# Kernel tuning notes

Hardware: AMD Instinct MI355X
Metric: run time of the kernel (lower is better)

The kernel has to match this reference:

```python
import jax, jax.numpy as jnp
import numpy as np

NUM_HEADS = 8
BN_EPS = 1e-5


def setup_inputs() -> dict:
    key = jax.random.key(0)
    ks = jax.random.split(key, 8)
    B, Ct, Cs, H, W, E = 8, 256, 128, 32, 32, 256
    s = 0.05  # small init scale to keep softmax logits reasonable
    return {
        "tgt": jax.random.normal(ks[0], (B, Ct, H, W), jnp.float32),
        "src": jax.random.normal(ks[1], (B, Cs, H, W), jnp.float32),
        "kv_w": jax.random.normal(ks[2], (E, Cs), jnp.float32) * s,
        "in_proj_w": jax.random.normal(ks[3], (3 * E, E), jnp.float32) * s,
        "in_proj_b": jnp.zeros((3 * E,), jnp.float32),
        "out_proj_w": jax.random.normal(ks[4], (E, E), jnp.float32) * s,
        "out_proj_b": jnp.zeros((E,), jnp.float32),
        "fuse_w": jax.random.normal(ks[5], (Ct, E), jnp.float32) * s,
        "bn_gamma": jnp.ones((Ct,), jnp.float32),
        "bn_beta": jnp.zeros((Ct,), jnp.float32),
        "bn_mean": jnp.zeros((Ct,), jnp.float32),
        "bn_var": jnp.ones((Ct,), jnp.float32),
    }


def reference(tgt, src, kv_w, in_proj_w, in_proj_b, out_proj_w, out_proj_b,
              fuse_w, bn_gamma, bn_beta, bn_mean, bn_var):
    B, Ct, H, W = tgt.shape
    E = kv_w.shape[0]
    nH = NUM_HEADS
    hd = E // nH

    # q_proj is Identity (C_tgt == embed_dim); flatten spatial to tokens [B, Q, E]
    q_seq = tgt.reshape(B, Ct, H * W).transpose(0, 2, 1)
    # kv_proj: 1x1 conv == channel matmul; then flatten to [B, K, E]
    kv_map = jnp.einsum('bchw,ec->behw', src, kv_w)
    k_seq = kv_map.reshape(B, E, H * W).transpose(0, 2, 1)

    # nn.MultiheadAttention: packed in-projection
    Wq, Wk, Wv = in_proj_w[:E], in_proj_w[E:2 * E], in_proj_w[2 * E:]
    bq, bk, bv = in_proj_b[:E], in_proj_b[E:2 * E], in_proj_b[2 * E:]
    qp = (q_seq @ Wq.T + bq).reshape(B, -1, nH, hd).transpose(0, 2, 1, 3)  # [B,h,Q,d]
    kp = (k_seq @ Wk.T + bk).reshape(B, -1, nH, hd).transpose(0, 2, 1, 3)  # [B,h,K,d]
    vp = (k_seq @ Wv.T + bv).reshape(B, -1, nH, hd).transpose(0, 2, 1, 3)  # [B,h,K,d]

    scores = jnp.einsum('bhqd,bhkd->bhqk', qp, kp) / jnp.sqrt(jnp.float32(hd))
    attn = jax.nn.softmax(scores, axis=-1)  # [B,h,Q,K] (non-flash explicit path)

    ctx = jnp.einsum('bhqk,bhkd->bhqd', attn, vp)
    ctx = ctx.transpose(0, 2, 1, 3).reshape(B, -1, E)  # [B,Q,E]
    out_seq = ctx @ out_proj_w.T + out_proj_b

    # cached spatial key-attention map: mean over heads and queries -> [B,1,Hk,Wk]
    attn_map = attn.mean(axis=(1, 2)).reshape(B, 1, H, W)

    # back to map, fuse: 1x1 conv -> BN(eval) -> SiLU, then residual add
    out_map = out_seq.transpose(0, 2, 1).reshape(B, E, H, W)
    fused = jnp.einsum('behw,ce->bchw', out_map, fuse_w)
    inv = bn_gamma / jnp.sqrt(bn_var + BN_EPS)
    bn = (fused - bn_mean[None, :, None, None]) * inv[None, :, None, None] \
         + bn_beta[None, :, None, None]
    y = tgt + bn * jax.nn.sigmoid(bn)  # SiLU
    return y, attn_map
```

## Files before the change

kernel.cpp:

```cpp
#include <hip/hip_runtime.h>
#include <hip/hip_bf16.h>

typedef unsigned short u16;
typedef unsigned int u32;
typedef __attribute__((ext_vector_type(8))) short short8;
typedef __attribute__((ext_vector_type(4))) float f32x4;
typedef __attribute__((ext_vector_type(4))) unsigned short u16x4;
typedef __attribute__((ext_vector_type(4))) int i32x4;

static __device__ __forceinline__ u16 f2bf(float x) {
  __hip_bfloat16 b = __float2bfloat16(x);
  return *reinterpret_cast<u16*>(&b);
}
static __device__ __forceinline__ u32 fbits(float x) {
  union { float f; u32 u; } v; v.f = x; return v.u;
}
static __device__ __forceinline__ u32 pk_trunc(float lo, float hi) {
  return __builtin_amdgcn_perm(fbits(hi), fbits(lo), 0x07060302u);
}
static __device__ __forceinline__ void gl2lds16(const u16* g, u16* l) {
  __builtin_amdgcn_global_load_lds(
      (const __attribute__((address_space(1))) void*)g,
      (__attribute__((address_space(3))) void*)l, 16, 0, 0);
}

#define QSCALE2 (0.17677669529663687f * 1.4426950408889634f)

__global__ __launch_bounds__(256) void prep_xpose(
    const float* __restrict__ in_proj_w, const float* __restrict__ in_proj_b,
    const float* __restrict__ kv_w, const float* __restrict__ fuse_w,
    const float* __restrict__ out_proj_w, const float* __restrict__ out_proj_b,
    const float* __restrict__ gamma, const float* __restrict__ beta,
    const float* __restrict__ mean, const float* __restrict__ var,
    const float* __restrict__ tgt, const float* __restrict__ src,
    u16* __restrict__ WqB, u16* __restrict__ WkvB, u16* __restrict__ M2B,
    float* __restrict__ qbias, float2* __restrict__ bnpk,
    u16* __restrict__ tgtT, u16* __restrict__ srcT,
    float* __restrict__ attn_out) {
  if (blockIdx.x >= 1537) {
    int i = (blockIdx.x - 1537) * 256 + threadIdx.x;
    attn_out[i] = 0.f;
    return;
  }
  if (blockIdx.x < 769) {
    int idx = blockIdx.x * 256 + threadIdx.x;
    if (idx < 65536) {
      WqB[idx] = f2bf(in_proj_w[idx] * QSCALE2);
    } else if (idx < 131072) {
      int i = idx - 65536;
      int m = i >> 7, c = i & 127;
      const float* wrow = in_proj_w + (size_t)(256 + m) * 256;
      float s = 0.f;
      for (int e2 = 0; e2 < 256; ++e2) s += wrow[e2] * kv_w[e2 * 128 + c];
      WkvB[i] = f2bf(s);
    } else if (idx < 196608) {
      int i = idx - 131072;
      int c = i >> 8, e2 = i & 255;
      float s = 0.f;
      for (int e = 0; e < 256; ++e)
        s += fuse_w[c * 256 + e] * out_proj_w[e * 256 + e2];
      M2B[i] = f2bf(s);
    } else if (idx < 196864) {
      int c = idx - 196608;
      float fbv = 0.f;
      for (int e = 0; e < 256; ++e) fbv += fuse_w[c * 256 + e] * out_proj_b[e];
      float inv = gamma[c] * rsqrtf(var[c] + 1e-5f);
      bnpk[c] = make_float2(inv, (fbv - mean[c]) * inv + beta[c]);
      qbias[c] = in_proj_b[c] * QSCALE2;
    }
    return;
  }
  int i0 = blockIdx.x - 769;
  int b = i0 / 96, rem = i0 % 96;
  int by = rem >> 4, sb = (rem & 15) * 64;
  const float* X;
  u16* XT;
  int C, cb;
  if (by < 4) {
    X = tgt + (size_t)b * 256 * 1024;
    XT = tgtT + (size_t)b * 1024 * 256;
    C = 256;
    cb = by * 64;
  } else {
    X = src + (size_t)b * 128 * 1024;
    XT = srcT + (size_t)b * 1024 * 128;
    C = 128;
    cb = (by - 4) * 64;
  }
  int t = threadIdx.x;
  int c = cb + (t >> 4) * 4;
  int s = sb + (t & 15) * 4;
  const float* Xp = X + (size_t)c * 1024 + s;
  float4 r0 = *(const float4*)(Xp);
  float4 r1 = *(const float4*)(Xp + 1024);
  float4 r2 = *(const float4*)(Xp + 2048);
  float4 r3 = *(const float4*)(Xp + 3072);
  u16* XTp = XT + (size_t)s * C + c;
  u16x4 o;
  o[0] = f2bf(r0.x); o[1] = f2bf(r1.x); o[2] = f2bf(r2.x); o[3] = f2bf(r3.x);
  *(u16x4*)(XTp) = o;
  o[0] = f2bf(r0.y); o[1] = f2bf(r1.y); o[2] = f2bf(r2.y); o[3] = f2bf(r3.y);
  *(u16x4*)(XTp + C) = o;
  o[0] = f2bf(r0.z); o[1] = f2bf(r1.z); o[2] = f2bf(r2.z); o[3] = f2bf(r3.z);
  *(u16x4*)(XTp + 2 * C) = o;
  o[0] = f2bf(r0.w); o[1] = f2bf(r1.w); o[2] = f2bf(r2.w); o[3] = f2bf(r3.w);
  *(u16x4*)(XTp + 3 * C) = o;
}

__global__ __launch_bounds__(256, 4) void qkv_gemm(
    const u16* __restrict__ tgtT, const u16* __restrict__ srcT,
    const u16* __restrict__ WqB, const u16* __restrict__ WkvB,
    const float* __restrict__ qbias, const float* __restrict__ bkv,
    u16* __restrict__ QB, u16* __restrict__ KB, u16* __restrict__ VB) {
  __shared__ __align__(16) u16 Wl[64 * 32];
  __shared__ __align__(16) u16 Xl[128 * 32];
  int b = blockIdx.z, my = blockIdx.y, n0 = blockIdx.x * 128;
  bool isQ = my < 4;
  int m0 = isQ ? my * 64 : (my - 4) * 64;
  int Kd = isQ ? 256 : 128;
  const u16* Wp = isQ ? WqB : WkvB;
  const u16* Xp = isQ ? tgtT + (size_t)b * 1024 * 256
                      : srcT + (size_t)b * 1024 * 128;
  int t = threadIdx.x, wave = t >> 6, lane = t & 63;
  int lq = lane & 15, quad = lane >> 4;
  int srow = t >> 2, sseg = t & 3;
  f32x4 acc[4][2];
#pragma unroll
  for (int mt = 0; mt < 4; ++mt)
#pragma unroll
    for (int nt = 0; nt < 2; ++nt) acc[mt][nt] = (f32x4){0.f, 0.f, 0.f, 0.f};

  for (int k0 = 0; k0 < Kd; k0 += 32) {
    __syncthreads();
    gl2lds16(&Wp[(size_t)(m0 + srow) * Kd + k0 + sseg * 8], &Wl[wave * 512]);
    gl2lds16(&Xp[(size_t)(n0 + srow) * Kd + k0 + sseg * 8], &Xl[wave * 512]);
    gl2lds16(&Xp[(size_t)(n0 + 64 + srow) * Kd + k0 + sseg * 8],
             &Xl[2048 + wave * 512]);
    __syncthreads();
    short8 af[4], bf[2];
#pragma unroll
    for (int mt = 0; mt < 4; ++mt)
      af[mt] = *(const short8*)&Wl[(mt * 16 + lq) * 32 + quad * 8];
#pragma unroll
    for (int nt = 0; nt < 2; ++nt)
      bf[nt] = *(const short8*)&Xl[(wave * 32 + nt * 16 + lq) * 32 + quad * 8];
#pragma unroll
    for (int mt = 0; mt < 4; ++mt)
#pragma unroll
      for (int nt = 0; nt < 2; ++nt)
        acc[mt][nt] = __builtin_amdgcn_mfma_f32_16x16x32_bf16(af[mt], bf[nt],
                                                              acc[mt][nt], 0, 0, 0);
  }
  if (isQ) {
#pragma unroll
    for (int mt = 0; mt < 4; ++mt) {
      int e = m0 + mt * 16 + quad * 4;
      f32x4 bi = *(const f32x4*)&qbias[e];
      int hh = e >> 5, d0 = e & 31;
#pragma unroll
      for (int nt = 0; nt < 2; ++nt) {
        int n = n0 + wave * 32 + nt * 16 + lq;
        u16x4 pk;
#pragma unroll
        for (int r = 0; r < 4; ++r) pk[r] = f2bf(acc[mt][nt][r] + bi[r]);
        *(u16x4*)&QB[((size_t)(b * 8 + hh) * 1024 + n) * 32 + d0] = pk;
      }
    }
  } else {
#pragma unroll
    for (int mt = 0; mt < 4; ++mt) {
      int m = m0 + mt * 16 + quad * 4;
      f32x4 bi = *(const f32x4*)&bkv[m];
#pragma unroll
      for (int nt = 0; nt < 2; ++nt) {
        int n = n0 + wave * 32 + nt * 16 + lq;
        if (m < 256) {
          int hh = m >> 5, d = m & 31;
          u16x4 pk;
#pragma unroll
          for (int r = 0; r < 4; ++r) pk[r] = f2bf(acc[mt][nt][r] + bi[r]);
          *(u16x4*)&KB[((size_t)(b * 8 + hh) * 1024 + n) * 32 + d] = pk;
        } else {
          int e = m - 256;
#pragma unroll
          for (int r = 0; r < 4; ++r)
            VB[((size_t)b * 256 + e + r) * 1024 + n] = f2bf(acc[mt][nt][r] + bi[r]);
        }
      }
    }
  }
}

__global__ __launch_bounds__(256, 4) void attn_passA(
    const u16* __restrict__ QB, const u16* __restrict__ KB,
    const u16* __restrict__ VB, u16* __restrict__ ctxB,
    float* __restrict__ linv_ws) {
  __shared__ __align__(16) u16 Klds[256 * 32];
  __shared__ __align__(16) u16 Vlds[8 * 1056];
  int bidx = blockIdx.x;
  int pair = bidx & 63, q0 = (bidx >> 6) * 64;
  int b = pair >> 3, h = pair & 7;
  int t = threadIdx.x, wave = t >> 6, lane = t & 63;
  int lq = lane & 15, quad = lane >> 4;
  int srow = t >> 2, sseg = t & 3;

  const u16* Qb = QB + (size_t)pair * 1024 * 32;
  const u16* Kb = KB + (size_t)pair * 1024 * 32;
  const u16* Vb = VB + (size_t)(b * 256 + h * 32) * 1024;

  int myq = q0 + wave * 16 + lq;
  short8 qf = *(const short8*)(Qb + (size_t)myq * 32 + quad * 8);

  const f32x4 zf = (f32x4){0.f, 0.f, 0.f, 0.f};
  f32x4 O0 = zf, O1 = zf;
  float lsum = 0.f;
  int keyA = ((lq >> 2) << 3) | (lq & 3);

  for (int c0 = 0; c0 < 1024; c0 += 256) {
    __syncthreads();
#pragma unroll
    for (int i = 0; i < 4; ++i)
      gl2lds16(Kb + (size_t)(c0 + i * 64 + srow) * 32 + sseg * 8,
               &Klds[i * 2048 + wave * 512]);
#pragma unroll
    for (int i = 0; i < 2; ++i) {
      int g = wave * 2 + i;
#pragma unroll
      for (int j = 0; j < 2; ++j) {
        int d = g * 4 + j * 2 + (lane >> 5);
        gl2lds16(Vb + (size_t)d * 1024 + c0 + (lane & 31) * 8,
                 &Vlds[g * 1056 + j * 512]);
      }
    }
    __syncthreads();
#pragma unroll
    for (int pr = 0; pr < 8; ++pr) {
      short8 kf0 = *(const short8*)&Klds[(pr * 32 + keyA) * 32 + quad * 8];
      short8 kf1 = *(const short8*)&Klds[(pr * 32 + keyA + 4) * 32 + quad * 8];
      f32x4 s0 = __builtin_amdgcn_mfma_f32_16x16x32_bf16(kf0, qf, zf, 0, 0, 0);
      f32x4 s1 = __builtin_amdgcn_mfma_f32_16x16x32_bf16(kf1, qf, zf, 0, 0, 0);
      f32x4 e0, e1;
#pragma unroll
      for (int r = 0; r < 4; ++r) {
        e0[r] = exp2f(s0[r]);
        e1[r] = exp2f(s1[r]);
      }
      lsum += (e0[0] + e0[1]) + (e0[2] + e0[3]) +
              (e1[0] + e1[1]) + (e1[2] + e1[3]);
      i32x4 pi;
      pi[0] = (int)pk_trunc(e0[0], e0[1]);
      pi[1] = (int)pk_trunc(e0[2], e0[3]);
      pi[2] = (int)pk_trunc(e1[0], e1[1]);
      pi[3] = (int)pk_trunc(e1[2], e1[3]);
      short8 pf = *(short8*)&pi;
      short8 vf0 = *(const short8*)&Vlds[(lq >> 2) * 1056 + (lq & 3) * 256 +
                                         pr * 32 + quad * 8];
      short8 vf1 = *(const short8*)&Vlds[(4 + (lq >> 2)) * 1056 + (lq & 3) * 256 +
                                         pr * 32 + quad * 8];
      O0 = __builtin_amdgcn_mfma_f32_16x16x32_bf16(vf0, pf, O0, 0, 0, 0);
      O1 = __builtin_amdgcn_mfma_f32_16x16x32_bf16(vf1, pf, O1, 0, 0, 0);
    }
  }

  lsum += __shfl_xor(lsum, 16);
  lsum += __shfl_xor(lsum, 32);
  float linv = 1.f / lsum;

  u16x4 pk0, pk1;
#pragma unroll
  for (int r = 0; r < 4; ++r) {
    pk0[r] = f2bf(O0[r] * linv);
    pk1[r] = f2bf(O1[r] * linv);
  }
  u16* crow = ctxB + ((size_t)b * 1024 + myq) * 256 + h * 32 + quad * 4;
  *(u16x4*)crow = pk0;
  *(u16x4*)(crow + 16) = pk1;
  if (quad == 0) linv_ws[(size_t)pair * 1024 + myq] = linv;
}

__global__ __launch_bounds__(256, 4) void colsum_kernel(
    const u16* __restrict__ QB, const u16* __restrict__ KB,
    const float* __restrict__ linv_ws, float* __restrict__ attn_out) {
  __shared__ __align__(16) u16 Klds[64 * 32];
  int bidx = blockIdx.x;
  int pair = bidx & 63, k0 = (bidx >> 6) * 64;
  int b = pair >> 3;
  int t = threadIdx.x, wave = t >> 6, lane = t & 63;
  int lq = lane & 15, quad = lane >> 4;
  int srow = t >> 2, sseg = t & 3;

  const u16* Qb = QB + (size_t)pair * 1024 * 32;
  const u16* Kb = KB + (size_t)pair * 1024 * 32;
  const float* lvp = linv_ws + (size_t)pair * 1024;

  gl2lds16(Kb + (size_t)(k0 + srow) * 32 + sseg * 8, &Klds[wave * 512]);
  __syncthreads();

  short8 kf[4];
#pragma unroll
  for (int nt = 0; nt < 4; ++nt)
    kf[nt] = *(const short8*)&Klds[(nt * 16 + lq) * 32 + quad * 8];

  const f32x4 zf = (f32x4){0.f, 0.f, 0.f, 0.f};
  float cs[4] = {0.f, 0.f, 0.f, 0.f};
  for (int g = 0; g < 16; ++g) {
    int qg = g * 64 + wave * 16;
    short8 qf = *(const short8*)(Qb + (size_t)(qg + lq) * 32 + quad * 8);
    f32x4 lv = *(const f32x4*)&lvp[qg + quad * 4];
#pragma unroll
    for (int nt = 0; nt < 4; ++nt) {
      f32x4 s = __builtin_amdgcn_mfma_f32_16x16x32_bf16(qf, kf[nt], zf, 0, 0, 0);
      cs[nt] += exp2f(s[0]) * lv[0] + exp2f(s[1]) * lv[1] +
                exp2f(s[2]) * lv[2] + exp2f(s[3]) * lv[3];
    }
  }
#pragma unroll
  for (int nt = 0; nt < 4; ++nt) {
    float v = cs[nt];
    v += __shfl_xor(v, 16);
    v += __shfl_xor(v, 32);
    if (quad == 0)
      atomicAdd(&attn_out[b * 1024 + k0 + nt * 16 + lq], v * (1.f / 8192.f));
  }
}

__global__ __launch_bounds__(256, 4) void fused_out(
    const u16* __restrict__ M2B, const u16* __restrict__ ctxB,
    const float* __restrict__ tgt, const float2* __restrict__ bnpk,
    float* __restrict__ y) {
  __shared__ __align__(16) u16 Al[64 * 32];
  __shared__ __align__(16) u16 Bl[64 * 32];
  int b = blockIdx.z, c0 = blockIdx.y * 64, s0 = blockIdx.x * 64;
  int t = threadIdx.x, wave = t >> 6, lane = t & 63;
  int lq = lane & 15, quad = lane >> 4;
  int srow = t >> 2, sseg = t & 3;
  f32x4 acc[4];
#pragma unroll
  for (int mt = 0; mt < 4; ++mt) acc[mt] = (f32x4){0.f, 0.f, 0.f, 0.f};

  for (int k0 = 0; k0 < 256; k0 += 32) {
    __syncthreads();
    gl2lds16(&M2B[(size_t)(c0 + srow) * 256 + k0 + sseg * 8], &Al[wave * 512]);
    gl2lds16(&ctxB[((size_t)b * 1024 + s0 + srow) * 256 + k0 + sseg * 8],
             &Bl[wave * 512]);
    __syncthreads();
    short8 bf = *(const short8*)&Bl[(wave * 16 + lq) * 32 + quad * 8];
    short8 af[4];
#pragma unroll
    for (int mt = 0; mt < 4; ++mt)
      af[mt] = *(const short8*)&Al[(mt * 16 + lq) * 32 + quad * 8];
#pragma unroll
    for (int mt = 0; mt < 4; ++mt)
      acc[mt] = __builtin_amdgcn_mfma_f32_16x16x32_bf16(af[mt], bf, acc[mt], 0, 0, 0);
  }
  int s = s0 + wave * 16 + lq;
#pragma unroll
  for (int mt = 0; mt < 4; ++mt) {
#pragma unroll
    for (int r = 0; r < 4; ++r) {
      int c = c0 + mt * 16 + quad * 4 + r;
      float2 p = bnpk[c];
      float bn = acc[mt][r] * p.x + p.y;
      float sig = 1.f / (1.f + __expf(-bn));
      size_t idx = ((size_t)b * 256 + c) * 1024 + s;
      y[idx] = tgt[idx] + bn * sig;
    }
  }
}

extern "C" void kernel_launch(void* const* d_in, const int* in_sizes, int n_in,
                              void* d_out, int out_size, void* d_ws, size_t ws_size,
                              hipStream_t stream) {
  const float* tgt = (const float*)d_in[0];
  const float* src = (const float*)d_in[1];
  const float* kv_w = (const float*)d_in[2];
  const float* in_proj_w = (const float*)d_in[3];
  const float* in_proj_b = (const float*)d_in[4];
  const float* out_proj_w = (const float*)d_in[5];
  const float* out_proj_b = (const float*)d_in[6];
  const float* fuse_w = (const float*)d_in[7];
  const float* bn_gamma = (const float*)d_in[8];
  const float* bn_beta = (const float*)d_in[9];
  const float* bn_mean = (const float*)d_in[10];
  const float* bn_var = (const float*)d_in[11];

  char* W = (char*)d_ws;
  u16* WqB = (u16*)W;
  u16* WkvB = (u16*)(W + 131072);
  u16* M2B = (u16*)(W + 262144);
  float* qbias = (float*)(W + 393216);
  float2* bnpk = (float2*)(W + 394240);
  u16* tgtT = (u16*)(W + 397312);
  u16* srcT = tgtT + 2097152;
  u16* QB = srcT + 1048576;
  u16* KB = QB + 2097152;
  u16* VB = KB + 2097152;
  u16* ctxB = VB + 2097152;
  float* linv_ws = (float*)(ctxB + 2097152);

  float* y = (float*)d_out;
  float* attn_out = y + 2097152;

  prep_xpose<<<1569, 256, 0, stream>>>(in_proj_w, in_proj_b, kv_w, fuse_w,
                                       out_proj_w, out_proj_b, bn_gamma, bn_beta,
                                       bn_mean, bn_var, tgt, src,
                                       WqB, WkvB, M2B, qbias, bnpk, tgtT, srcT,
                                       attn_out);
  qkv_gemm<<<dim3(8, 12, 8), 256, 0, stream>>>(tgtT, srcT, WqB, WkvB, qbias,
                                               in_proj_b + 256, QB, KB, VB);
  attn_passA<<<1024, 256, 0, stream>>>(QB, KB, VB, ctxB, linv_ws);
  colsum_kernel<<<1024, 256, 0, stream>>>(QB, KB, linv_ws, attn_out);
  fused_out<<<dim3(16, 4, 8), 256, 0, stream>>>(M2B, ctxB, tgt, bnpk, y);
}
```

Before: 158.9 us.

## Double-buffer LDS staging in GEMMs and attention, merge colsum and output kernels

Adds double-buffered LDS tiles to qkv_gemm, attn_passA and the output GEMM, so the next chunk's global-to-LDS loads are issued before computing on the current chunk. Each K-loop now needs one barrier per step instead of two. attn_passA now processes 128-key chunks instead of 256. The independent colsum and fused output kernels are merged into one launch with 1536 blocks, split by block index, which removes a launch and lets the two workloads run concurrently. The costs are more LDS per block and a shared-memory footprint sized for the larger of the two branches.

```diff
diff --git a/kernel.cpp b/kernel.cpp
--- a/kernel.cpp
+++ b/kernel.cpp
@@ -112,8 +112,8 @@
     const u16* __restrict__ WqB, const u16* __restrict__ WkvB,
     const float* __restrict__ qbias, const float* __restrict__ bkv,
     u16* __restrict__ QB, u16* __restrict__ KB, u16* __restrict__ VB) {
-  __shared__ __align__(16) u16 Wl[64 * 32];
-  __shared__ __align__(16) u16 Xl[128 * 32];
+  __shared__ __align__(16) u16 Wl[2][64 * 32];
+  __shared__ __align__(16) u16 Xl[2][128 * 32];
   int b = blockIdx.z, my = blockIdx.y, n0 = blockIdx.x * 128;
   bool isQ = my < 4;
   int m0 = isQ ? my * 64 : (my - 4) * 64;
@@ -130,39 +130,50 @@
 #pragma unroll
     for (int nt = 0; nt < 2; ++nt) acc[mt][nt] = (f32x4){0.f, 0.f, 0.f, 0.f};
 
-  for (int k0 = 0; k0 < Kd; k0 += 32) {
+  int nk = Kd >> 5;
+  gl2lds16(&Wp[(size_t)(m0 + srow) * Kd + sseg * 8], &Wl[0][wave * 512]);
+  gl2lds16(&Xp[(size_t)(n0 + srow) * Kd + sseg * 8], &Xl[0][wave * 512]);
+  gl2lds16(&Xp[(size_t)(n0 + 64 + srow) * Kd + sseg * 8],
+           &Xl[0][2048 + wave * 512]);
+  __syncthreads();
+  for (int kk = 0; kk < nk; ++kk) {
+    int bsel = kk & 1;
+    if (kk + 1 < nk) {
+      int k0 = (kk + 1) << 5;
+      gl2lds16(&Wp[(size_t)(m0 + srow) * Kd + k0 + sseg * 8],
+               &Wl[bsel ^ 1][wave * 512]);
+      gl2lds16(&Xp[(size_t)(n0 + srow) * Kd + k0 + sseg * 8],
+               &Xl[bsel ^ 1][wave * 512]);
+      gl2lds16(&Xp[(size_t)(n0 + 64 + srow) * Kd + k0 + sseg * 8],
+               &Xl[bsel ^ 1][2048 + wave * 512]);
+    }
+    short8 af[4], bfx[2];
+#pragma unroll
+    for (int mt = 0; mt < 4; ++mt)
+      af[mt] = *(const short8*)&Wl[bsel][(mt * 16 + lq) * 32 + quad * 8];
+#pragma unroll
+    for (int nt = 0; nt < 2; ++nt)
+      bfx[nt] = *(const short8*)&Xl[bsel][(wave * 32 + nt * 16 + lq) * 32 + quad * 8];
+#pragma unroll
+    for (int mt = 0; mt < 4; ++mt)
+#pragma unroll
+      for (int nt = 0; nt < 2; ++nt)
+        acc[mt][nt] = __builtin_amdgcn_mfma_f32_16x16x32_bf16(af[mt], bfx[nt],
+                                                              acc[mt][nt], 0, 0, 0);
     __syncthreads();
-    gl2lds16(&Wp[(size_t)(m0 + srow) * Kd + k0 + sseg * 8], &Wl[wave * 512]);
-    gl2lds16(&Xp[(size_t)(n0 + srow) * Kd + k0 + sseg * 8], &Xl[wave * 512]);
-    gl2lds16(&Xp[(size_t)(n0 + 64 + srow) * Kd + k0 + sseg * 8],
-             &Xl[2048 + wave * 512]);
-    __syncthreads();
-    short8 af[4], bf[2];
-#pragma unroll
-    for (int mt = 0; mt < 4; ++mt)
-      af[mt] = *(const short8*)&Wl[(mt * 16 + lq) * 32 + quad * 8];
-#pragma unroll
-    for (int nt = 0; nt < 2; ++nt)
-      bf[nt] = *(const short8*)&Xl[(wave * 32 + nt * 16 + lq) * 32 + quad * 8];
-#pragma unroll
-    for (int mt = 0; mt < 4; ++mt)
-#pragma unroll
-      for (int nt = 0; nt < 2; ++nt)
-        acc[mt][nt] = __builtin_amdgcn_mfma_f32_16x16x32_bf16(af[mt], bf[nt],
-                                                              acc[mt][nt], 0, 0, 0);
   }
   if (isQ) {
 #pragma unroll
     for (int mt = 0; mt < 4; ++mt) {
       int e = m0 + mt * 16 + quad * 4;
-      f32x4 bi = *(const f32x4*)&qbias[e];
+      f32x4 bia = *(const f32x4*)&qbias[e];
       int hh = e >> 5, d0 = e & 31;
 #pragma unroll
       for (int nt = 0; nt < 2; ++nt) {
         int n = n0 + wave * 32 + nt * 16 + lq;
         u16x4 pk;
 #pragma unroll
-        for (int r = 0; r < 4; ++r) pk[r] = f2bf(acc[mt][nt][r] + bi[r]);
+        for (int r = 0; r < 4; ++r) pk[r] = f2bf(acc[mt][nt][r] + bia[r]);
         *(u16x4*)&QB[((size_t)(b * 8 + hh) * 1024 + n) * 32 + d0] = pk;
       }
     }
@@ -170,7 +181,7 @@
 #pragma unroll
     for (int mt = 0; mt < 4; ++mt) {
       int m = m0 + mt * 16 + quad * 4;
-      f32x4 bi = *(const f32x4*)&bkv[m];
+      f32x4 bia = *(const f32x4*)&bkv[m];
 #pragma unroll
       for (int nt = 0; nt < 2; ++nt) {
         int n = n0 + wave * 32 + nt * 16 + lq;
@@ -178,16 +189,32 @@
           int hh = m >> 5, d = m & 31;
           u16x4 pk;
 #pragma unroll
-          for (int r = 0; r < 4; ++r) pk[r] = f2bf(acc[mt][nt][r] + bi[r]);
+          for (int r = 0; r < 4; ++r) pk[r] = f2bf(acc[mt][nt][r] + bia[r]);
           *(u16x4*)&KB[((size_t)(b * 8 + hh) * 1024 + n) * 32 + d] = pk;
         } else {
           int e = m - 256;
 #pragma unroll
           for (int r = 0; r < 4; ++r)
-            VB[((size_t)b * 256 + e + r) * 1024 + n] = f2bf(acc[mt][nt][r] + bi[r]);
+            VB[((size_t)b * 256 + e + r) * 1024 + n] = f2bf(acc[mt][nt][r] + bia[r]);
         }
       }
     }
+  }
+}
+
+static __device__ __forceinline__ void stage_kv(
+    const u16* __restrict__ Kb, const u16* __restrict__ Vb, int c0,
+    u16* __restrict__ Kl, u16* __restrict__ Vl,
+    int wave, int lane, int srow, int sseg) {
+#pragma unroll
+  for (int i = 0; i < 2; ++i)
+    gl2lds16(Kb + (size_t)(c0 + i * 64 + srow) * 32 + sseg * 8,
+             Kl + i * 2048 + wave * 512);
+#pragma unroll
+  for (int i = 0; i < 2; ++i) {
+    int g = wave * 2 + i;
+    gl2lds16(Vb + (size_t)(g * 4 + (lane >> 4)) * 1024 + c0 + (lane & 15) * 8,
+             Vl + g * 544);
   }
 }
 
@@ -195,8 +222,8 @@
     const u16* __restrict__ QB, const u16* __restrict__ KB,
     const u16* __restrict__ VB, u16* __restrict__ ctxB,
     float* __restrict__ linv_ws) {
-  __shared__ __align__(16) u16 Klds[256 * 32];
-  __shared__ __align__(16) u16 Vlds[8 * 1056];
+  __shared__ __align__(16) u16 Klds[2][128 * 32];
+  __shared__ __align__(16) u16 Vlds[2][8 * 544];
   int bidx = blockIdx.x;
   int pair = bidx & 63, q0 = (bidx >> 6) * 64;
   int b = pair >> 3, h = pair & 7;
@@ -216,27 +243,17 @@
   float lsum = 0.f;
   int keyA = ((lq >> 2) << 3) | (lq & 3);
 
-  for (int c0 = 0; c0 < 1024; c0 += 256) {
-    __syncthreads();
-#pragma unroll
-    for (int i = 0; i < 4; ++i)
-      gl2lds16(Kb + (size_t)(c0 + i * 64 + srow) * 32 + sseg * 8,
-               &Klds[i * 2048 + wave * 512]);
-#pragma unroll
-    for (int i = 0; i < 2; ++i) {
-      int g = wave * 2 + i;
-#pragma unroll
-      for (int j = 0; j < 2; ++j) {
-        int d = g * 4 + j * 2 + (lane >> 5);
-        gl2lds16(Vb + (size_t)d * 1024 + c0 + (lane & 31) * 8,
-                 &Vlds[g * 1056 + j * 512]);
-      }
-    }
-    __syncthreads();
-#pragma unroll
-    for (int pr = 0; pr < 8; ++pr) {
-      short8 kf0 = *(const short8*)&Klds[(pr * 32 + keyA) * 32 + quad * 8];
-      short8 kf1 = *(const short8*)&Klds[(pr * 32 + keyA + 4) * 32 + quad * 8];
+  stage_kv(Kb, Vb, 0, Klds[0], Vlds[0], wave, lane, srow, sseg);
+  __syncthreads();
+  for (int cc = 0; cc < 8; ++cc) {
+    int bsel = cc & 1;
+    if (cc < 7)
+      stage_kv(Kb, Vb, (cc + 1) * 128, Klds[bsel ^ 1], Vlds[bsel ^ 1],
+               wave, lane, srow, sseg);
+#pragma unroll
+    for (int pr = 0; pr < 4; ++pr) {
+      short8 kf0 = *(const short8*)&Klds[bsel][(pr * 32 + keyA) * 32 + quad * 8];
+      short8 kf1 = *(const short8*)&Klds[bsel][(pr * 32 + keyA + 4) * 32 + quad * 8];
       f32x4 s0 = __builtin_amdgcn_mfma_f32_16x16x32_bf16(kf0, qf, zf, 0, 0, 0);
       f32x4 s1 = __builtin_amdgcn_mfma_f32_16x16x32_bf16(kf1, qf, zf, 0, 0, 0);
       f32x4 e0, e1;
@@ -253,13 +270,14 @@
       pi[2] = (int)pk_trunc(e1[0], e1[1]);
       pi[3] = (int)pk_trunc(e1[2], e1[3]);
       short8 pf = *(short8*)&pi;
-      short8 vf0 = *(const short8*)&Vlds[(lq >> 2) * 1056 + (lq & 3) * 256 +
-                                         pr * 32 + quad * 8];
-      short8 vf1 = *(const short8*)&Vlds[(4 + (lq >> 2)) * 1056 + (lq & 3) * 256 +
-                                         pr * 32 + quad * 8];
+      short8 vf0 = *(const short8*)&Vlds[bsel][(lq >> 2) * 544 + (lq & 3) * 128 +
+                                               pr * 32 + quad * 8];
+      short8 vf1 = *(const short8*)&Vlds[bsel][(4 + (lq >> 2)) * 544 + (lq & 3) * 128 +
+                                               pr * 32 + quad * 8];
       O0 = __builtin_amdgcn_mfma_f32_16x16x32_bf16(vf0, pf, O0, 0, 0, 0);
       O1 = __builtin_amdgcn_mfma_f32_16x16x32_bf16(vf1, pf, O1, 0, 0, 0);
     }
+    __syncthreads();
   }
 
   lsum += __shfl_xor(lsum, 16);
@@ -278,80 +296,85 @@
   if (quad == 0) linv_ws[(size_t)pair * 1024 + myq] = linv;
 }
 
-__global__ __launch_bounds__(256, 4) void colsum_kernel(
+__global__ __launch_bounds__(256, 4) void tail_kernel(
+    const u16* __restrict__ M2B, const u16* __restrict__ ctxB,
+    const float* __restrict__ tgt, const float2* __restrict__ bnpk,
+    float* __restrict__ y,
     const u16* __restrict__ QB, const u16* __restrict__ KB,
     const float* __restrict__ linv_ws, float* __restrict__ attn_out) {
-  __shared__ __align__(16) u16 Klds[64 * 32];
-  int bidx = blockIdx.x;
-  int pair = bidx & 63, k0 = (bidx >> 6) * 64;
-  int b = pair >> 3;
+  __shared__ __align__(16) u16 SH[8192];
   int t = threadIdx.x, wave = t >> 6, lane = t & 63;
   int lq = lane & 15, quad = lane >> 4;
   int srow = t >> 2, sseg = t & 3;
-
-  const u16* Qb = QB + (size_t)pair * 1024 * 32;
-  const u16* Kb = KB + (size_t)pair * 1024 * 32;
-  const float* lvp = linv_ws + (size_t)pair * 1024;
-
-  gl2lds16(Kb + (size_t)(k0 + srow) * 32 + sseg * 8, &Klds[wave * 512]);
+  const f32x4 zf = (f32x4){0.f, 0.f, 0.f, 0.f};
+
+  if (blockIdx.x >= 512) {
+    int bidx = blockIdx.x - 512;
+    int pair = bidx & 63, k0 = (bidx >> 6) * 64;
+    int b = pair >> 3;
+    const u16* Qb = QB + (size_t)pair * 1024 * 32;
+    const u16* Kb = KB + (size_t)pair * 1024 * 32;
+    const float* lvp = linv_ws + (size_t)pair * 1024;
+
+    gl2lds16(Kb + (size_t)(k0 + srow) * 32 + sseg * 8, &SH[wave * 512]);
+    __syncthreads();
+
+    short8 kf[4];
+#pragma unroll
+    for (int nt = 0; nt < 4; ++nt)
+      kf[nt] = *(const short8*)&SH[(nt * 16 + lq) * 32 + quad * 8];
+
+    float cs[4] = {0.f, 0.f, 0.f, 0.f};
+    for (int g = 0; g < 16; ++g) {
+      int qg = g * 64 + wave * 16;
+      short8 qf = *(const short8*)(Qb + (size_t)(qg + lq) * 32 + quad * 8);
+      f32x4 lv = *(const f32x4*)&lvp[qg + quad * 4];
+#pragma unroll
+      for (int nt = 0; nt < 4; ++nt) {
+        f32x4 s = __builtin_amdgcn_mfma_f32_16x16x32_bf16(qf, kf[nt], zf, 0, 0, 0);
+        cs[nt] += exp2f(s[0]) * lv[0] + exp2f(s[1]) * lv[1] +
+                  exp2f(s[2]) * lv[2] + exp2f(s[3]) * lv[3];
+      }
+    }
+#pragma unroll
+    for (int nt = 0; nt < 4; ++nt) {
+      float v = cs[nt];
+      v += __shfl_xor(v, 16);
+      v += __shfl_xor(v, 32);
+      if (quad == 0)
+        atomicAdd(&attn_out[b * 1024 + k0 + nt * 16 + lq], v * (1.f / 8192.f));
+    }
+    return;
+  }
+
+  int ii = blockIdx.x;
+  int b = ii >> 6, c0 = ((ii >> 4) & 3) * 64, s0 = (ii & 15) * 64;
+  f32x4 acc[4];
+#pragma unroll
+  for (int mt = 0; mt < 4; ++mt) acc[mt] = zf;
+
+  gl2lds16(&M2B[(size_t)(c0 + srow) * 256 + sseg * 8], &SH[wave * 512]);
+  gl2lds16(&ctxB[((size_t)b * 1024 + s0 + srow) * 256 + sseg * 8],
+           &SH[4096 + wave * 512]);
   __syncthreads();
-
-  short8 kf[4];
-#pragma unroll
-  for (int nt = 0; nt < 4; ++nt)
-    kf[nt] = *(const short8*)&Klds[(nt * 16 + lq) * 32 + quad * 8];
-
-  const f32x4 zf = (f32x4){0.f, 0.f, 0.f, 0.f};
-  float cs[4] = {0.f, 0.f, 0.f, 0.f};
-  for (int g = 0; g < 16; ++g) {
-    int qg = g * 64 + wave * 16;
-    short8 qf = *(const short8*)(Qb + (size_t)(qg + lq) * 32 + quad * 8);
-    f32x4 lv = *(const f32x4*)&lvp[qg + quad * 4];
-#pragma unroll
-    for (int nt = 0; nt < 4; ++nt) {
-      f32x4 s = __builtin_amdgcn_mfma_f32_16x16x32_bf16(qf, kf[nt], zf, 0, 0, 0);
-      cs[nt] += exp2f(s[0]) * lv[0] + exp2f(s[1]) * lv[1] +
-                exp2f(s[2]) * lv[2] + exp2f(s[3]) * lv[3];
-    }
-  }
-#pragma unroll
-  for (int nt = 0; nt < 4; ++nt) {
-    float v = cs[nt];
-    v += __shfl_xor(v, 16);
-    v += __shfl_xor(v, 32);
-    if (quad == 0)
-      atomicAdd(&attn_out[b * 1024 + k0 + nt * 16 + lq], v * (1.f / 8192.f));
-  }
-}
-
-__global__ __launch_bounds__(256, 4) void fused_out(
-    const u16* __restrict__ M2B, const u16* __restrict__ ctxB,
-    const float* __restrict__ tgt, const float2* __restrict__ bnpk,
-    float* __restrict__ y) {
-  __shared__ __align__(16) u16 Al[64 * 32];
-  __shared__ __align__(16) u16 Bl[64 * 32];
-  int b = blockIdx.z, c0 = blockIdx.y * 64, s0 = blockIdx.x * 64;
-  int t = threadIdx.x, wave = t >> 6, lane = t & 63;
-  int lq = lane & 15, quad = lane >> 4;
-  int srow = t >> 2, sseg = t & 3;
-  f32x4 acc[4];
-#pragma unroll
-  for (int mt = 0; mt < 4; ++mt) acc[mt] = (f32x4){0.f, 0.f, 0.f, 0.f};
-
-  for (int k0 = 0; k0 < 256; k0 += 32) {
+  for (int kk = 0; kk < 8; ++kk) {
+    int bsel = kk & 1;
+    if (kk < 7) {
+      int k0 = (kk + 1) << 5;
+      gl2lds16(&M2B[(size_t)(c0 + srow) * 256 + k0 + sseg * 8],
+               &SH[(bsel ^ 1) * 2048 + wave * 512]);
+      gl2lds16(&ctxB[((size_t)b * 1024 + s0 + srow) * 256 + k0 + sseg * 8],
+               &SH[4096 + (bsel ^ 1) * 2048 + wave * 512]);
+    }
+    short8 bfx = *(const short8*)&SH[4096 + bsel * 2048 + (wave * 16 + lq) * 32 + quad * 8];
+    short8 af[4];
+#pragma unroll
+    for (int mt = 0; mt < 4; ++mt)
+      af[mt] = *(const short8*)&SH[bsel * 2048 + (mt * 16 + lq) * 32 + quad * 8];
+#pragma unroll
+    for (int mt = 0; mt < 4; ++mt)
+      acc[mt] = __builtin_amdgcn_mfma_f32_16x16x32_bf16(af[mt], bfx, acc[mt], 0, 0, 0);
     __syncthreads();
-    gl2lds16(&M2B[(size_t)(c0 + srow) * 256 + k0 + sseg * 8], &Al[wave * 512]);
-    gl2lds16(&ctxB[((size_t)b * 1024 + s0 + srow) * 256 + k0 + sseg * 8],
-             &Bl[wave * 512]);
-    __syncthreads();
-    short8 bf = *(const short8*)&Bl[(wave * 16 + lq) * 32 + quad * 8];
-    short8 af[4];
-#pragma unroll
-    for (int mt = 0; mt < 4; ++mt)
-      af[mt] = *(const short8*)&Al[(mt * 16 + lq) * 32 + quad * 8];
-#pragma unroll
-    for (int mt = 0; mt < 4; ++mt)
-      acc[mt] = __builtin_amdgcn_mfma_f32_16x16x32_bf16(af[mt], bf, acc[mt], 0, 0, 0);
   }
   int s = s0 + wave * 16 + lq;
 #pragma unroll
@@ -409,6 +432,6 @@
   qkv_gemm<<<dim3(8, 12, 8), 256, 0, stream>>>(tgtT, srcT, WqB, WkvB, qbias,
                                                in_proj_b + 256, QB, KB, VB);
   attn_passA<<<1024, 256, 0, stream>>>(QB, KB, VB, ctxB, linv_ws);
-  colsum_kernel<<<1024, 256, 0, stream>>>(QB, KB, linv_ws, attn_out);
-  fused_out<<<dim3(16, 4, 8), 256, 0, stream>>>(M2B, ctxB, tgt, bnpk, y);
-}
+  tail_kernel<<<1536, 256, 0, stream>>>(M2B, ctxB, tgt, bnpk, y,
+                                        QB, KB, linv_ws, attn_out);
+}
```

Measured after the change: 158.8 us. Within noise of the previous version (-0.0%).
